# Performance work log

Measured on AMD Instinct MI355X. Metric: run time of the kernel, lower is better.

## Reference

```python
import jax, jax.numpy as jnp
import numpy as np

NEG = -1000000000.0

def setup_inputs() -> dict:
    key = jax.random.key(0)
    k1, k2 = jax.random.split(key)
    N, D, K = 8192, 4096, 64
    z = jax.random.normal(k1, (N, D), dtype=jnp.float32)
    W = jax.random.normal(k2, (K, D), dtype=jnp.float32) * (1.0 / np.sqrt(D))
    b = jnp.zeros((K,), dtype=jnp.float32)
    return {"z": z, "W": W, "b": b, "k": 2}

def reference(z, W, b, k):
    # logits: [N, K]
    logits = jnp.einsum('nd,kd->nk', z, W) + b
    _, topk_idx = jax.lax.top_k(logits, k)  # [N, k]
    N = logits.shape[0]
    rows = jnp.arange(N)[:, None]
    mask = jnp.zeros_like(logits).at[rows, topk_idx].set(1.0)
    sparse_logits = logits + NEG * (1.0 - mask)
    alpha = jax.nn.softmax(sparse_logits, axis=-1)
    return alpha
```

## Files before the change

### kernel.cpp

```cpp
#include <hip/hip_runtime.h>
#include <math.h>


typedef _Float16 f16x8 __attribute__((ext_vector_type(8)));
typedef _Float16 f16x4 __attribute__((ext_vector_type(4)));
typedef float    f32x4 __attribute__((ext_vector_type(4)));

constexpr int D_DIM  = 4096;
constexpr int K_DIM  = 64;
constexpr int BM     = 128;
constexpr int KQ     = 16;
constexpr int KRANGE = D_DIM / KQ;
constexpr int BLOCK  = 512;
constexpr int BSTR   = 264;

__global__ __launch_bounds__(256) void prep_w(
    const float* __restrict__ W, _Float16* __restrict__ Wf0,
    _Float16* __restrict__ Wf1)
{
    int f = blockIdx.x * 256 + threadIdx.x;
    const float4 v = *(const float4*)(W + (long)f * 4);
    const float* p = (const float*)&v;
    f16x4 h, l;
#pragma unroll
    for (int j = 0; j < 4; ++j) {
        _Float16 hh = (_Float16)p[j];
        h[j] = hh;
        l[j] = (_Float16)((p[j] - (float)hh) * 2048.0f);
    }
    *(f16x4*)(Wf0 + (long)f * 4) = h;
    *(f16x4*)(Wf1 + (long)f * 4) = l;
}

__global__ __launch_bounds__(BLOCK, 4) void gemm_zreg(
    const float* __restrict__ z, const _Float16* __restrict__ Wf0,
    const _Float16* __restrict__ Wf1, float* __restrict__ part, int N)
{
    __shared__ __align__(16) _Float16 Bs[2][K_DIM][BSTR];

    const int tid  = threadIdx.x;
    const int lane = tid & 63;
    const int wv   = tid >> 6;
    const int m16  = lane & 15;
    const int quad = lane >> 4;

    const int rgrp  = blockIdx.x >> 4;
    const int kq    = blockIdx.x & 15;
    const long m0   = (long)rgrp * BM;
    const int kbase = kq * KRANGE;

    const float* zp = z + (m0 + wv * 16 + m16) * (long)D_DIM + kbase;
    float4 za[16];
#pragma unroll
    for (int s = 0; s < 8; ++s) {
        za[s * 2 + 0] = *(const float4*)(zp + s * 32 + quad * 8);
        za[s * 2 + 1] = *(const float4*)(zp + s * 32 + quad * 8 + 4);
    }

#pragma unroll
    for (int i = 0; i < 8; ++i) {
        int f  = tid + i * BLOCK;
        int p  = f >> 11;
        int rr = (f >> 5) & 63;
        int c  = f & 31;
        const _Float16* src = (p ? Wf1 : Wf0) + (long)rr * D_DIM + kbase + c * 8;
        *(f16x8*)&Bs[p][rr][c * 8] = *(const f16x8*)src;
    }
    __syncthreads();

    f32x4 acch[4], accl[4];
#pragma unroll
    for (int nt = 0; nt < 4; ++nt) {
        acch[nt] = (f32x4){0.f, 0.f, 0.f, 0.f};
        accl[nt] = (f32x4){0.f, 0.f, 0.f, 0.f};
    }

#pragma unroll
    for (int s = 0; s < 8; ++s) {
        f16x8 ah, al;
        const float* pz = (const float*)&za[s * 2];
#pragma unroll
        for (int j = 0; j < 8; ++j) {
            _Float16 hh = (_Float16)pz[j];
            ah[j] = hh;
            al[j] = (_Float16)((pz[j] - (float)hh) * 2048.0f);
        }
        const int ko = s * 32 + quad * 8;
#pragma unroll
        for (int nt = 0; nt < 4; ++nt) {
            const f16x8 bh = *(const f16x8*)&Bs[0][nt * 16 + m16][ko];
            const f16x8 bl = *(const f16x8*)&Bs[1][nt * 16 + m16][ko];
            accl[nt] = __builtin_amdgcn_mfma_f32_16x16x32_f16(al, bh, accl[nt], 0, 0, 0);
            accl[nt] = __builtin_amdgcn_mfma_f32_16x16x32_f16(ah, bl, accl[nt], 0, 0, 0);
            acch[nt] = __builtin_amdgcn_mfma_f32_16x16x32_f16(ah, bh, acch[nt], 0, 0, 0);
        }
    }

#pragma unroll
    for (int nt = 0; nt < 4; ++nt) {
#pragma unroll
        for (int r = 0; r < 4; ++r) {
            long row = m0 + wv * 16 + quad * 4 + r;
            part[((long)kq * N + row) * K_DIM + nt * 16 + m16] =
                acch[nt][r] + accl[nt][r] * 4.8828125e-4f;
        }
    }
}

constexpr int RG2  = 32;
constexpr int BLK2 = 256;

__global__ __launch_bounds__(BLK2) void reduce_topk(
    const float* __restrict__ part, const float* __restrict__ bias,
    float* __restrict__ out, int N)
{
    __shared__ float lg[RG2][K_DIM + 1];
    __shared__ float sa1[RG2], sa2[RG2];
    __shared__ int   si1[RG2], si2[RG2];

    const int tid = threadIdx.x;
    const long r0 = (long)blockIdx.x * RG2;

#pragma unroll
    for (int i = 0; i < (RG2 * K_DIM) / (BLK2 * 4); ++i) {
        int f = tid + i * BLK2, r = f >> 4, c4 = (f & 15) * 4;
        float4 s = *(const float4*)(part + (r0 + r) * K_DIM + c4);
#pragma unroll
        for (int q = 1; q < KQ; ++q) {
            const float4 v = *(const float4*)(part + ((long)q * N + r0 + r) * K_DIM + c4);
            s.x += v.x; s.y += v.y; s.z += v.z; s.w += v.w;
        }
        const float4 bv = *(const float4*)(bias + c4);
        lg[r][c4 + 0] = s.x + bv.x;
        lg[r][c4 + 1] = s.y + bv.y;
        lg[r][c4 + 2] = s.z + bv.z;
        lg[r][c4 + 3] = s.w + bv.w;
    }
    __syncthreads();

    if (tid < RG2) {
        float m1 = -INFINITY, m2 = -INFINITY;
        int i1 = 0, i2 = 0;
        for (int j = 0; j < K_DIM; ++j) {
            float v = lg[tid][j];
            if (v > m1)      { m2 = m1; i2 = i1; m1 = v; i1 = j; }
            else if (v > m2) { m2 = v; i2 = j; }
        }
        float e2  = expf(m2 - m1);
        float inv = 1.f / (1.f + e2);
        sa1[tid] = inv; sa2[tid] = e2 * inv;
        si1[tid] = i1;  si2[tid] = i2;
    }
    __syncthreads();

    float* obase = out + r0 * K_DIM;
#pragma unroll
    for (int i = 0; i < (RG2 * K_DIM) / (BLK2 * 4); ++i) {
        int f = tid + i * BLK2, r = f >> 4, j = (f & 15) * 4;
        int i1 = si1[r], i2 = si2[r];
        float a1 = sa1[r], a2 = sa2[r];
        float4 v;
        v.x = (j + 0 == i1) ? a1 : ((j + 0 == i2) ? a2 : 0.f);
        v.y = (j + 1 == i1) ? a1 : ((j + 1 == i2) ? a2 : 0.f);
        v.z = (j + 2 == i1) ? a1 : ((j + 2 == i2) ? a2 : 0.f);
        v.w = (j + 3 == i1) ? a1 : ((j + 3 == i2) ? a2 : 0.f);
        *(float4*)(obase + (long)r * K_DIM + j) = v;
    }
}

extern "C" void kernel_launch(void* const* d_in, const int* in_sizes, int n_in,
                              void* d_out, int out_size, void* d_ws, size_t ws_size,
                              hipStream_t stream) {
    const float* z = (const float*)d_in[0];
    const float* W = (const float*)d_in[1];
    const float* b = (const float*)d_in[2];
    float* out  = (float*)d_out;
    const int N = in_sizes[0] / D_DIM;

    float*    part = (float*)d_ws;
    _Float16* Wf0  = (_Float16*)((char*)d_ws + ((size_t)64 << 20));
    _Float16* Wf1  = Wf0 + (size_t)K_DIM * D_DIM;

    prep_w     <<<dim3((K_DIM * D_DIM / 4) / 256), dim3(256), 0, stream>>>(W, Wf0, Wf1);
    gemm_zreg  <<<dim3((N / BM) * KQ), dim3(BLOCK), 0, stream>>>(z, Wf0, Wf1, part, N);
    reduce_topk<<<dim3(N / RG2),       dim3(BLK2), 0, stream>>>(part, b, out, N);
}
```

Measured before the change: 210.9 us.

## Fuse W prep, GEMM, and top-k softmax into one register-prefetched kernel

Replaces the three-kernel pipeline (W fp16 split, split-K GEMM writing partials, reduce+topk) with a single kernel where each block owns 32 rows and loops over the full D in 256-wide chunks. z and W chunks are prefetched into registers and double-buffered into LDS, W is split to hi/lo fp16 on the fly, and top-2 softmax is done in-block. This removes the partial-sum round trip through global memory and two extra launches. In exchange, every block re-reads and re-converts all of W (64x4096) and synchronizes four times per chunk pair. The grid drops to 256 blocks, which may leave the device underoccupied.

```diff
diff --git a/kernel.cpp b/kernel.cpp
--- a/kernel.cpp
+++ b/kernel.cpp
@@ -6,139 +6,116 @@
 typedef _Float16 f16x4 __attribute__((ext_vector_type(4)));
 typedef float    f32x4 __attribute__((ext_vector_type(4)));
 
-constexpr int D_DIM  = 4096;
-constexpr int K_DIM  = 64;
-constexpr int BM     = 128;
-constexpr int KQ     = 16;
-constexpr int KRANGE = D_DIM / KQ;
-constexpr int BLOCK  = 512;
-constexpr int BSTR   = 264;
+constexpr int D_DIM = 4096;
+constexpr int K_DIM = 64;
+constexpr int BM    = 32;
+constexpr int BLOCK = 512;
+constexpr int CK    = 256;
+constexpr int NCH   = D_DIM / CK;
+constexpr int WSTR  = 264;
+constexpr int ZSTR  = 260;
 
-__global__ __launch_bounds__(256) void prep_w(
-    const float* __restrict__ W, _Float16* __restrict__ Wf0,
-    _Float16* __restrict__ Wf1)
+#define ISSUE(c, zr, wr) do {                                                  \
+    const float* zc_ = z + m0 * D_DIM + (c) * CK;                              \
+    _Pragma("unroll")                                                          \
+    for (int i = 0; i < 4; ++i)                                                \
+        zr[i] = *(const f32x4*)(zc_ + (long)(wv + i * 8) * D_DIM + lane * 4);  \
+    const float* wc_ = W + (c) * CK;                                           \
+    _Pragma("unroll")                                                          \
+    for (int i = 0; i < 8; ++i)                                                \
+        wr[i] = *(const f32x4*)(wc_ + (long)(wv + i * 8) * D_DIM + lane * 4);  \
+} while (0)
+
+#define PARK(zr, wr) do {                                                      \
+    _Pragma("unroll")                                                          \
+    for (int i = 0; i < 4; ++i)                                                \
+        *(f32x4*)&zs[wv + i * 8][lane * 4] = zr[i];                            \
+    _Pragma("unroll")                                                          \
+    for (int i = 0; i < 8; ++i) {                                              \
+        f16x4 h_, l_;                                                          \
+        _Pragma("unroll")                                                      \
+        for (int j = 0; j < 4; ++j) {                                          \
+            _Float16 hh = (_Float16)wr[i][j];                                  \
+            h_[j] = hh;                                                        \
+            l_[j] = (_Float16)((wr[i][j] - (float)hh) * 2048.0f);              \
+        }                                                                      \
+        *(f16x4*)&Ws[0][wv + i * 8][lane * 4] = h_;                            \
+        *(f16x4*)&Ws[1][wv + i * 8][lane * 4] = l_;                            \
+    }                                                                          \
+} while (0)
+
+#define COMPUTE() do {                                                         \
+    _Pragma("unroll")                                                          \
+    for (int s = 0; s < CK / 32; ++s) {                                        \
+        const int ko = s * 32 + quad * 8;                                      \
+        const f32x4 a0 = *(const f32x4*)&zs[mt * 16 + m16][ko];                \
+        const f32x4 a1 = *(const f32x4*)&zs[mt * 16 + m16][ko + 4];            \
+        f16x8 ah, al;                                                          \
+        _Pragma("unroll")                                                      \
+        for (int j = 0; j < 4; ++j) {                                          \
+            _Float16 h0 = (_Float16)a0[j];                                     \
+            ah[j]     = h0;                                                    \
+            al[j]     = (_Float16)((a0[j] - (float)h0) * 2048.0f);             \
+            _Float16 h1 = (_Float16)a1[j];                                     \
+            ah[j + 4] = h1;                                                    \
+            al[j + 4] = (_Float16)((a1[j] - (float)h1) * 2048.0f);             \
+        }                                                                      \
+        const f16x8 bh = *(const f16x8*)&Ws[0][nt * 16 + m16][ko];             \
+        const f16x8 bl = *(const f16x8*)&Ws[1][nt * 16 + m16][ko];             \
+        accl = __builtin_amdgcn_mfma_f32_16x16x32_f16(al, bh, accl, 0, 0, 0);  \
+        accl = __builtin_amdgcn_mfma_f32_16x16x32_f16(ah, bl, accl, 0, 0, 0);  \
+        acch = __builtin_amdgcn_mfma_f32_16x16x32_f16(ah, bh, acch, 0, 0, 0);  \
+    }                                                                          \
+} while (0)
+
+__global__ __launch_bounds__(BLOCK, 2) void router_fused(
+    const float* __restrict__ z, const float* __restrict__ W,
+    const float* __restrict__ bias, float* __restrict__ out)
 {
-    int f = blockIdx.x * 256 + threadIdx.x;
-    const float4 v = *(const float4*)(W + (long)f * 4);
-    const float* p = (const float*)&v;
-    f16x4 h, l;
-#pragma unroll
-    for (int j = 0; j < 4; ++j) {
-        _Float16 hh = (_Float16)p[j];
-        h[j] = hh;
-        l[j] = (_Float16)((p[j] - (float)hh) * 2048.0f);
-    }
-    *(f16x4*)(Wf0 + (long)f * 4) = h;
-    *(f16x4*)(Wf1 + (long)f * 4) = l;
-}
-
-__global__ __launch_bounds__(BLOCK, 4) void gemm_zreg(
-    const float* __restrict__ z, const _Float16* __restrict__ Wf0,
-    const _Float16* __restrict__ Wf1, float* __restrict__ part, int N)
-{
-    __shared__ __align__(16) _Float16 Bs[2][K_DIM][BSTR];
+    __shared__ __align__(16) _Float16 Ws[2][K_DIM][WSTR];
+    __shared__ __align__(16) float    zs[BM][ZSTR];
+    __shared__ float lg[BM][K_DIM + 1];
+    __shared__ float sa1[BM], sa2[BM];
+    __shared__ int   si1[BM], si2[BM];
 
     const int tid  = threadIdx.x;
     const int lane = tid & 63;
-    const int wv   = tid >> 6;
     const int m16  = lane & 15;
     const int quad = lane >> 4;
+    const int wv   = tid >> 6;
+    const int mt   = wv >> 2;
+    const int nt   = wv & 3;
 
-    const int rgrp  = blockIdx.x >> 4;
-    const int kq    = blockIdx.x & 15;
-    const long m0   = (long)rgrp * BM;
-    const int kbase = kq * KRANGE;
+    const long m0 = (long)blockIdx.x * BM;
 
-    const float* zp = z + (m0 + wv * 16 + m16) * (long)D_DIM + kbase;
-    float4 za[16];
-#pragma unroll
-    for (int s = 0; s < 8; ++s) {
-        za[s * 2 + 0] = *(const float4*)(zp + s * 32 + quad * 8);
-        za[s * 2 + 1] = *(const float4*)(zp + s * 32 + quad * 8 + 4);
+    f32x4 zrA[4], wrA[8], zrB[4], wrB[8];
+    f32x4 acch = {0.f, 0.f, 0.f, 0.f};
+    f32x4 accl = {0.f, 0.f, 0.f, 0.f};
+
+    ISSUE(0, zrA, wrA);
+
+#pragma unroll 1
+    for (int cc = 0; cc < NCH / 2; ++cc) {
+        if (cc) __syncthreads();
+        PARK(zrA, wrA);
+        ISSUE(2 * cc + 1, zrB, wrB);
+        __syncthreads();
+        COMPUTE();
+        __syncthreads();
+        PARK(zrB, wrB);
+        if (2 * cc + 2 < NCH) ISSUE(2 * cc + 2, zrA, wrA);
+        __syncthreads();
+        COMPUTE();
     }
 
+    const float bv = bias[nt * 16 + m16];
 #pragma unroll
-    for (int i = 0; i < 8; ++i) {
-        int f  = tid + i * BLOCK;
-        int p  = f >> 11;
-        int rr = (f >> 5) & 63;
-        int c  = f & 31;
-        const _Float16* src = (p ? Wf1 : Wf0) + (long)rr * D_DIM + kbase + c * 8;
-        *(f16x8*)&Bs[p][rr][c * 8] = *(const f16x8*)src;
-    }
+    for (int r = 0; r < 4; ++r)
+        lg[mt * 16 + quad * 4 + r][nt * 16 + m16] =
+            acch[r] + accl[r] * 4.8828125e-4f + bv;
     __syncthreads();
 
-    f32x4 acch[4], accl[4];
-#pragma unroll
-    for (int nt = 0; nt < 4; ++nt) {
-        acch[nt] = (f32x4){0.f, 0.f, 0.f, 0.f};
-        accl[nt] = (f32x4){0.f, 0.f, 0.f, 0.f};
-    }
-
-#pragma unroll
-    for (int s = 0; s < 8; ++s) {
-        f16x8 ah, al;
-        const float* pz = (const float*)&za[s * 2];
-#pragma unroll
-        for (int j = 0; j < 8; ++j) {
-            _Float16 hh = (_Float16)pz[j];
-            ah[j] = hh;
-            al[j] = (_Float16)((pz[j] - (float)hh) * 2048.0f);
-        }
-        const int ko = s * 32 + quad * 8;
-#pragma unroll
-        for (int nt = 0; nt < 4; ++nt) {
-            const f16x8 bh = *(const f16x8*)&Bs[0][nt * 16 + m16][ko];
-            const f16x8 bl = *(const f16x8*)&Bs[1][nt * 16 + m16][ko];
-            accl[nt] = __builtin_amdgcn_mfma_f32_16x16x32_f16(al, bh, accl[nt], 0, 0, 0);
-            accl[nt] = __builtin_amdgcn_mfma_f32_16x16x32_f16(ah, bl, accl[nt], 0, 0, 0);
-            acch[nt] = __builtin_amdgcn_mfma_f32_16x16x32_f16(ah, bh, acch[nt], 0, 0, 0);
-        }
-    }
-
-#pragma unroll
-    for (int nt = 0; nt < 4; ++nt) {
-#pragma unroll
-        for (int r = 0; r < 4; ++r) {
-            long row = m0 + wv * 16 + quad * 4 + r;
-            part[((long)kq * N + row) * K_DIM + nt * 16 + m16] =
-                acch[nt][r] + accl[nt][r] * 4.8828125e-4f;
-        }
-    }
-}
-
-constexpr int RG2  = 32;
-constexpr int BLK2 = 256;
-
-__global__ __launch_bounds__(BLK2) void reduce_topk(
-    const float* __restrict__ part, const float* __restrict__ bias,
-    float* __restrict__ out, int N)
-{
-    __shared__ float lg[RG2][K_DIM + 1];
-    __shared__ float sa1[RG2], sa2[RG2];
-    __shared__ int   si1[RG2], si2[RG2];
-
-    const int tid = threadIdx.x;
-    const long r0 = (long)blockIdx.x * RG2;
-
-#pragma unroll
-    for (int i = 0; i < (RG2 * K_DIM) / (BLK2 * 4); ++i) {
-        int f = tid + i * BLK2, r = f >> 4, c4 = (f & 15) * 4;
-        float4 s = *(const float4*)(part + (r0 + r) * K_DIM + c4);
-#pragma unroll
-        for (int q = 1; q < KQ; ++q) {
-            const float4 v = *(const float4*)(part + ((long)q * N + r0 + r) * K_DIM + c4);
-            s.x += v.x; s.y += v.y; s.z += v.z; s.w += v.w;
-        }
-        const float4 bv = *(const float4*)(bias + c4);
-        lg[r][c4 + 0] = s.x + bv.x;
-        lg[r][c4 + 1] = s.y + bv.y;
-        lg[r][c4 + 2] = s.z + bv.z;
-        lg[r][c4 + 3] = s.w + bv.w;
-    }
-    __syncthreads();
-
-    if (tid < RG2) {
+    if (tid < BM) {
         float m1 = -INFINITY, m2 = -INFINITY;
         int i1 = 0, i2 = 0;
         for (int j = 0; j < K_DIM; ++j) {
@@ -153,18 +130,17 @@
     }
     __syncthreads();
 
-    float* obase = out + r0 * K_DIM;
-#pragma unroll
-    for (int i = 0; i < (RG2 * K_DIM) / (BLK2 * 4); ++i) {
-        int f = tid + i * BLK2, r = f >> 4, j = (f & 15) * 4;
-        int i1 = si1[r], i2 = si2[r];
-        float a1 = sa1[r], a2 = sa2[r];
-        float4 v;
-        v.x = (j + 0 == i1) ? a1 : ((j + 0 == i2) ? a2 : 0.f);
-        v.y = (j + 1 == i1) ? a1 : ((j + 1 == i2) ? a2 : 0.f);
-        v.z = (j + 2 == i1) ? a1 : ((j + 2 == i2) ? a2 : 0.f);
-        v.w = (j + 3 == i1) ? a1 : ((j + 3 == i2) ? a2 : 0.f);
-        *(float4*)(obase + (long)r * K_DIM + j) = v;
+    {
+        const int r  = tid >> 4;
+        const int c4 = (tid & 15) * 4;
+        const int i1 = si1[r], i2 = si2[r];
+        const float a1 = sa1[r], a2 = sa2[r];
+        f32x4 v;
+        v[0] = (c4 + 0 == i1) ? a1 : ((c4 + 0 == i2) ? a2 : 0.f);
+        v[1] = (c4 + 1 == i1) ? a1 : ((c4 + 1 == i2) ? a2 : 0.f);
+        v[2] = (c4 + 2 == i1) ? a1 : ((c4 + 2 == i2) ? a2 : 0.f);
+        v[3] = (c4 + 3 == i1) ? a1 : ((c4 + 3 == i2) ? a2 : 0.f);
+        *(f32x4*)(out + (m0 + r) * K_DIM + c4) = v;
     }
 }
 
@@ -176,12 +152,7 @@
     const float* b = (const float*)d_in[2];
     float* out  = (float*)d_out;
     const int N = in_sizes[0] / D_DIM;
+    (void)d_ws; (void)ws_size; (void)n_in; (void)out_size;
 
-    float*    part = (float*)d_ws;
-    _Float16* Wf0  = (_Float16*)((char*)d_ws + ((size_t)64 << 20));
-    _Float16* Wf1  = Wf0 + (size_t)K_DIM * D_DIM;
-
-    prep_w     <<<dim3((K_DIM * D_DIM / 4) / 256), dim3(256), 0, stream>>>(W, Wf0, Wf1);
-    gemm_zreg  <<<dim3((N / BM) * KQ), dim3(BLOCK), 0, stream>>>(z, Wf0, Wf1, part, N);
-    reduce_topk<<<dim3(N / RG2),       dim3(BLK2), 0, stream>>>(part, b, out, N);
+    router_fused<<<dim3(N / BM), dim3(BLOCK), 0, stream>>>(z, W, b, out);
 }
```

After: 213.4 us. About the same (+1.2%).
